# Optimization experiments

Hardware: AMD Instinct MI355X
Metric: run time of the kernel (lower is better)

## Reference

```python
import jax, jax.numpy as jnp
import numpy as np

B, IN, OUT, LAT, HID = 65536, 1, 512, 128, 2048
COEFFS = (IN + 1) * OUT * 2  # (in+1)*out*n_harmonics*n_eig = 2048

def setup_inputs() -> dict:
    key = jax.random.key(0)
    k = jax.random.split(key, 6)
    x = jax.random.normal(k[0], (B, IN + 1 + LAT), dtype=jnp.float32)
    fc1_w = jax.random.normal(k[1], (LAT, HID), dtype=jnp.float32) * (1.0 / np.sqrt(LAT))
    fc1_b = jax.random.normal(k[2], (HID,), dtype=jnp.float32) * 0.02
    fc2_w = jax.random.normal(k[3], (HID, COEFFS), dtype=jnp.float32) * (1.0 / np.sqrt(HID))
    fc2_b = jax.random.normal(k[4], (COEFFS,), dtype=jnp.float32) * 0.02
    dil = jnp.ones((4,), dtype=jnp.float32)      # dilation1..4
    shift_p = jnp.zeros((4,), dtype=jnp.float32)  # shift1..4
    return {"x": x, "fc1_w": fc1_w, "fc1_b": fc1_b, "fc2_w": fc2_w,
            "fc2_b": fc2_b, "dil": dil, "shift_p": shift_p}

def reference(x, fc1_w, fc1_b, fc2_w, fc2_b, dil, shift_p):
    s = x[-1, IN]                       # scalar time of last sample
    inp = x[:, :IN]                     # [B, 1]
    z = x[:, -LAT:]                     # [B, LAT]
    # CoeffDecoder: tanh MLP
    h = jnp.tanh(z @ fc1_w + fc1_b)     # [B, HID]
    coeffs = (h @ fc2_w + fc2_b).reshape(B, (IN + 1) * OUT, 2)
    # aew trig basis Bin (2x4) has only 4 nonzeros; X.sum(2) == coeffs @ Bin.sum(axis=1)
    t = s * dil + shift_p               # [4]
    v = jnp.stack([jnp.cos(t[0]) + jnp.cos(t[2]),
                   jnp.sin(t[1]) + jnp.sin(t[3])])  # [2] = row-sums of Bin
    w = coeffs @ v                      # [B, (IN+1)*OUT]
    weight = w[:, :IN * OUT].reshape(B, IN, OUT)
    bias = w[:, IN * OUT:(IN + 1) * OUT]
    weighted = jnp.einsum('bi,bio->bo', inp, weight)  # bmm([B,1,1],[B,1,OUT]).squeeze(1)
    return weighted + bias              # [B, OUT]
```

## Files before the change

kernel.cpp:

```cpp
#include <hip/hip_runtime.h>
#include <hip/hip_bf16.h>
#include <stddef.h>

#define NB   65536
#define XC   130
#define LATD 128
#define HIDD 2048
#define JC   1024
#define OC   512
#define BAND 16384
#define WBM  256
#define WBN  256
#define BK   64
#define NKT  32

typedef __bf16 bf16_t;
typedef bf16_t bf16x4 __attribute__((ext_vector_type(4)));
typedef bf16_t bf16x8 __attribute__((ext_vector_type(8)));
typedef float  f32x4  __attribute__((ext_vector_type(4)));

typedef __attribute__((address_space(1))) const unsigned char ga_u8;
typedef __attribute__((address_space(3))) unsigned char ls_u8;

__device__ __forceinline__ void dma16(const void* g, void* l) {
  __builtin_amdgcn_global_load_lds((ga_u8*)g, (ls_u8*)l, 16, 0, 0);
}

__global__ void prep_fc1(const float* __restrict__ fc1w, bf16_t* __restrict__ fc1wT) {
  int t = blockIdx.x * blockDim.x + threadIdx.x;
  int k = t & (LATD - 1);
  int n = t >> 7;
  fc1wT[(size_t)n * LATD + k] = (bf16_t)fc1w[(size_t)k * HIDD + n];
}

__global__ void prep_fc2(const float* __restrict__ x, const float* __restrict__ fc2w,
                         const float* __restrict__ fc2b, const float* __restrict__ dil,
                         const float* __restrict__ shp, bf16_t* __restrict__ w2pT,
                         float* __restrict__ b2p) {
  int t = blockIdx.x * blockDim.x + threadIdx.x;
  int k = t & (HIDD - 1);
  int c = t >> 11;
  float s  = x[(size_t)(NB - 1) * XC + 1];
  float t0 = s * dil[0] + shp[0];
  float t1 = s * dil[1] + shp[1];
  float t2 = s * dil[2] + shp[2];
  float t3 = s * dil[3] + shp[3];
  float v0 = cosf(t0) + cosf(t2);
  float v1 = sinf(t1) + sinf(t3);
  int jj = ((c >> 5) * 16 + (c & 15)) + (((c >> 4) & 1) << 9);
  float w0 = fc2w[(size_t)k * 2048 + 2 * jj];
  float w1 = fc2w[(size_t)k * 2048 + 2 * jj + 1];
  w2pT[(size_t)c * HIDD + k] = (bf16_t)(w0 * v0 + w1 * v1);
  if (k == 0) b2p[c] = fc2b[2 * jj] * v0 + fc2b[2 * jj + 1] * v1;
}

__global__ __launch_bounds__(512) void h_kernel(
    const float* __restrict__ x, const float* __restrict__ fc1b,
    const bf16_t* __restrict__ fc1wT, bf16_t* __restrict__ h, int band)
{
  const int t   = threadIdx.x;
  const int w   = t >> 6;
  const int l   = t & 63;
  const int lhi = l >> 4;
  const int llo = l & 15;
  const size_t b0 = (size_t)band * BAND + (size_t)blockIdx.x * 64;
  const int hb  = w & 1;
  const int gb  = (w >> 1) * 16;
  const size_t row_l = (size_t)blockIdx.x * 64 + gb + llo;

  bf16x8 za[4];
  {
    const float* zsrc = x + (b0 + gb + llo) * XC + 2;
#pragma unroll
    for (int ks = 0; ks < 4; ++ks) {
      bf16x8 pk;
#pragma unroll
      for (int i = 0; i < 4; ++i) {
        float2 f = *(const float2*)(zsrc + ks * 32 + lhi * 8 + 2 * i);
        pk[2 * i]     = (bf16_t)f.x;
        pk[2 * i + 1] = (bf16_t)f.y;
      }
      za[ks] = pk;
    }
  }

  auto loadA = [&](bf16x8 (&A)[4], int c) {
    const bf16_t* base = fc1wT + (size_t)(c * 32 + hb * 16 + llo) * LATD + lhi * 8;
#pragma unroll
    for (int ks = 0; ks < 4; ++ks) A[ks] = *(const bf16x8*)(base + ks * 32);
  };
  auto compute = [&](int c, bf16x8 (&A)[4]) {
    f32x4 c1 = {};
#pragma unroll
    for (int ks = 0; ks < 4; ++ks)
      c1 = __builtin_amdgcn_mfma_f32_16x16x32_bf16(A[ks], za[ks], c1, 0, 0, 0);
    float4 fb = *(const float4*)(fc1b + c * 32 + hb * 16 + lhi * 4);
    bf16x4 pk;
#pragma unroll
    for (int r = 0; r < 4; ++r) {
      float pre = c1[r] + ((const float*)&fb)[r];
      float e   = __builtin_amdgcn_exp2f(pre * 2.88539008177792681f);
      float th  = 1.0f - 2.0f * __builtin_amdgcn_rcpf(e + 1.0f);
      pk[r] = (bf16_t)th;
    }
    *(bf16x4*)(h + row_l * HIDD + c * 32 + hb * 16 + lhi * 4) = pk;
  };

  bf16x8 A0[4], A1[4], A2[4], A3[4];
  loadA(A0, 0); loadA(A1, 1); loadA(A2, 2); loadA(A3, 3);
  for (int c = 0; c < 64; c += 4) {
    compute(c,     A0);  loadA(A0, c + 4 < 64 ? c + 4 : 63);
    compute(c + 1, A1);  loadA(A1, c + 5 < 64 ? c + 5 : 63);
    compute(c + 2, A2);  loadA(A2, c + 6 < 64 ? c + 6 : 63);
    compute(c + 3, A3);  loadA(A3, c + 7 < 64 ? c + 7 : 63);
  }
}

__global__ __launch_bounds__(512, 2) void wag_main(
    const float* __restrict__ x, const bf16_t* __restrict__ hband,
    const bf16_t* __restrict__ w2pT, const float* __restrict__ b2p,
    float* __restrict__ out, int band)
{
  __shared__ bf16_t Ab[2][WBM * BK];
  __shared__ bf16_t Bb[2][WBN * BK];
  __shared__ float  inp_lds[WBM];

  const int t   = threadIdx.x;
  const int w   = t >> 6;
  const int l   = t & 63;
  const int lhi = l >> 4;
  const int llo = l & 15;

  const int n   = blockIdx.x;
  const int s_  = n >> 3;
  const int rt  = (n & 7) * 8 + (s_ >> 2);
  const int cg  = s_ & 3;
  const int hr0 = rt * WBM;
  const size_t bg0 = (size_t)band * BAND + hr0;
  const int bc  = cg * WBN;
  const int mrb = (w >> 2) * 128;
  const int ncb = (w & 3) * 64;

  if (t < WBM) inp_lds[t] = x[(bg0 + t) * XC];

  f32x4 acc[8][4] = {};

  auto stageA = [&](int kt) {
    bf16_t* dst = Ab[kt & 1];
#pragma unroll
    for (int q = 0; q < 4; ++q) {
      int idx  = q * 512 + t;
      int row  = idx >> 3, slot = idx & 7;
      const char* src = (const char*)(hband + (size_t)(hr0 + row) * HIDD + kt * BK
                                      + ((slot ^ (row & 7)) * 8));
      dma16(src, (char*)dst + idx * 16);
    }
  };
  auto stageB = [&](int kt) {
    bf16_t* dst = Bb[kt & 1];
#pragma unroll
    for (int q = 0; q < 4; ++q) {
      int idx  = q * 512 + t;
      int col  = idx >> 3, slot = idx & 7;
      const char* src = (const char*)(w2pT + (size_t)(bc + col) * HIDD + kt * BK
                                      + ((slot ^ (col & 7)) * 8));
      dma16(src, (char*)dst + idx * 16);
    }
  };

  auto KSTEP = [&](int kt) {
    const char* Ab_ = (const char*)Ab[kt & 1];
    const char* Bb_ = (const char*)Bb[kt & 1];
#pragma unroll
    for (int ks2 = 0; ks2 < 2; ++ks2) {
      bf16x8 b[4];
#pragma unroll
      for (int j = 0; j < 4; ++j) {
        int col = ncb + j * 16 + llo;
        b[j] = *(const bf16x8*)(Bb_ + col * 128 + ((ks2 * 64 + lhi * 16) ^ ((col & 7) << 4)));
      }
#pragma unroll
      for (int rh = 0; rh < 2; ++rh) {
        bf16x8 a[4];
#pragma unroll
        for (int i = 0; i < 4; ++i) {
          int row = mrb + rh * 64 + i * 16 + llo;
          a[i] = *(const bf16x8*)(Ab_ + row * 128 + ((ks2 * 64 + lhi * 16) ^ ((row & 7) << 4)));
        }
        __builtin_amdgcn_s_setprio(1);
#pragma unroll
        for (int j = 0; j < 4; ++j)
#pragma unroll
          for (int i = 0; i < 4; ++i)
            acc[rh * 4 + i][j] =
                __builtin_amdgcn_mfma_f32_16x16x32_bf16(a[i], b[j], acc[rh * 4 + i][j], 0, 0, 0);
        __builtin_amdgcn_s_setprio(0);
      }
    }
  };

  stageA(0); stageB(0);
  __syncthreads();
  for (int kt = 0; kt < NKT - 1; ++kt) {
    stageA(kt + 1); stageB(kt + 1);
    asm volatile("s_waitcnt vmcnt(8)" ::: "memory");
    __builtin_amdgcn_s_barrier();
    KSTEP(kt);
    asm volatile("s_waitcnt lgkmcnt(0)" ::: "memory");
    __builtin_amdgcn_s_barrier();
  }
  asm volatile("s_waitcnt vmcnt(0)" ::: "memory");
  __builtin_amdgcn_s_barrier();
  KSTEP(NKT - 1);

#pragma unroll
  for (int p = 0; p < 2; ++p) {
    int cw = bc + ncb + p * 32 + llo;
    float bw = b2p[cw];
    float bb = b2p[cw + 16];
    int oc = (bc + ncb + p * 32) / 2 + llo;
#pragma unroll
    for (int fi = 0; fi < 8; ++fi) {
#pragma unroll
      for (int r = 0; r < 4; ++r) {
        int row = mrb + fi * 16 + lhi * 4 + r;
        float wv = acc[fi][2 * p][r] + bw;
        float bv = acc[fi][2 * p + 1][r] + bb;
        out[(bg0 + row) * OC + oc] = inp_lds[row] * wv + bv;
      }
    }
  }
}

extern "C" void kernel_launch(void* const* d_in, const int* in_sizes, int n_in,
                              void* d_out, int out_size, void* d_ws, size_t ws_size,
                              hipStream_t stream) {
  const float* x    = (const float*)d_in[0];
  const float* fc1w = (const float*)d_in[1];
  const float* fc1b = (const float*)d_in[2];
  const float* fc2w = (const float*)d_in[3];
  const float* fc2b = (const float*)d_in[4];
  const float* dil  = (const float*)d_in[5];
  const float* shp  = (const float*)d_in[6];
  float* out = (float*)d_out;

  bf16_t* fc1wT = (bf16_t*)d_ws;
  bf16_t* w2pT  = fc1wT + (size_t)HIDD * LATD;
  float*  b2p   = (float*)(w2pT + (size_t)JC * HIDD);
  bf16_t* hband = (bf16_t*)((char*)d_ws + (8u << 20));

  prep_fc1<<<(HIDD * LATD) / 256, 256, 0, stream>>>(fc1w, fc1wT);
  prep_fc2<<<(JC * HIDD) / 256, 256, 0, stream>>>(x, fc2w, fc2b, dil, shp, w2pT, b2p);

  for (int band = 0; band < NB / BAND; ++band) {
    h_kernel<<<BAND / 64, 512, 0, stream>>>(x, fc1b, fc1wT, hband, band);
    wag_main<<<WBM == 256 ? (BAND / WBM) * (JC / WBN) : 0, 512, 0, stream>>>(
        x, hband, w2pT, b2p, out, band);
  }
}
```

Measured before the change: 570.5 us.

## Coalesce prep_fc2 via LDS transpose and stage h_kernel stores through LDS

prep_fc2 now loads fc2 weight tiles with coalesced reads into shared memory, then transposes them and writes vectorised bf16x8 rows of the folded weight matrix. Previously each thread did strided global reads. h_kernel is reorganised so each block handles 32 rows, and each wave covers a 512-wide slice of the hidden dimension. The tanh outputs go to a per-wave LDS tile first and are then written to global memory as full contiguous 16-byte row segments instead of scattered 8-byte stores. This adds LDS usage and a launch-bounds occupancy hint, and it reloads z for fewer rows per block.

```diff
diff --git a/kernel.cpp b/kernel.cpp
--- a/kernel.cpp
+++ b/kernel.cpp
@@ -33,13 +33,16 @@
   fc1wT[(size_t)n * LATD + k] = (bf16_t)fc1w[(size_t)k * HIDD + n];
 }
 
-__global__ void prep_fc2(const float* __restrict__ x, const float* __restrict__ fc2w,
-                         const float* __restrict__ fc2b, const float* __restrict__ dil,
-                         const float* __restrict__ shp, bf16_t* __restrict__ w2pT,
-                         float* __restrict__ b2p) {
-  int t = blockIdx.x * blockDim.x + threadIdx.x;
-  int k = t & (HIDD - 1);
-  int c = t >> 11;
+__global__ __launch_bounds__(256) void prep_fc2(
+    const float* __restrict__ x, const float* __restrict__ fc2w,
+    const float* __restrict__ fc2b, const float* __restrict__ dil,
+    const float* __restrict__ shp, bf16_t* __restrict__ w2pT,
+    float* __restrict__ b2p) {
+  __shared__ float tile[128 * 67];
+  const int t  = threadIdx.x;
+  const int g  = blockIdx.x;
+  const int k0 = blockIdx.y * 128;
+
   float s  = x[(size_t)(NB - 1) * XC + 1];
   float t0 = s * dil[0] + shp[0];
   float t1 = s * dil[1] + shp[1];
@@ -47,30 +50,58 @@
   float t3 = s * dil[3] + shp[3];
   float v0 = cosf(t0) + cosf(t2);
   float v1 = sinf(t1) + sinf(t3);
-  int jj = ((c >> 5) * 16 + (c & 15)) + (((c >> 4) & 1) << 9);
-  float w0 = fc2w[(size_t)k * 2048 + 2 * jj];
-  float w1 = fc2w[(size_t)k * 2048 + 2 * jj + 1];
-  w2pT[(size_t)c * HIDD + k] = (bf16_t)(w0 * v0 + w1 * v1);
-  if (k == 0) b2p[c] = fc2b[2 * jj] * v0 + fc2b[2 * jj + 1] * v1;
-}
-
-__global__ __launch_bounds__(512) void h_kernel(
+
+  {
+    int fi_ = t & 63, run = fi_ >> 5, fi = fi_ & 31, wv = t >> 6;
+#pragma unroll 8
+    for (int pass = 0; pass < 32; ++pass) {
+      int kr = pass * 4 + wv;
+      tile[kr * 67 + run * 32 + fi] =
+          fc2w[(size_t)(k0 + kr) * 2048 + run * 1024 + g * 32 + fi];
+    }
+  }
+  __syncthreads();
+
+  {
+    int cl = t >> 3, half = (cl >> 4) & 1, col16 = cl & 15;
+    int c = g * 32 + cl;
+    int pb = half * 32 + col16 * 2;
+    bf16x8 ov0, ov1;
+#pragma unroll
+    for (int kk = 0; kk < 16; ++kk) {
+      int k = (t & 7) * 16 + kk;
+      float f0 = tile[k * 67 + pb];
+      float f1 = tile[k * 67 + pb + 1];
+      bf16_t bv = (bf16_t)(f0 * v0 + f1 * v1);
+      if (kk < 8) ov0[kk] = bv; else ov1[kk - 8] = bv;
+    }
+    *(bf16x8*)(w2pT + (size_t)c * 2048 + k0 + (t & 7) * 16)     = ov0;
+    *(bf16x8*)(w2pT + (size_t)c * 2048 + k0 + (t & 7) * 16 + 8) = ov1;
+    if (blockIdx.y == 0 && (t & 7) == 0) {
+      int jj = g * 16 + col16 + (half << 9);
+      b2p[c] = fc2b[2 * jj] * v0 + fc2b[2 * jj + 1] * v1;
+    }
+  }
+}
+
+__global__ __launch_bounds__(512, 4) void h_kernel(
     const float* __restrict__ x, const float* __restrict__ fc1b,
     const bf16_t* __restrict__ fc1wT, bf16_t* __restrict__ h, int band)
 {
+  __shared__ char tile[8][16 * 528];
   const int t   = threadIdx.x;
   const int w   = t >> 6;
   const int l   = t & 63;
   const int lhi = l >> 4;
   const int llo = l & 15;
-  const size_t b0 = (size_t)band * BAND + (size_t)blockIdx.x * 64;
-  const int hb  = w & 1;
-  const int gb  = (w >> 1) * 16;
-  const size_t row_l = (size_t)blockIdx.x * 64 + gb + llo;
+  const size_t b0 = (size_t)band * BAND + (size_t)blockIdx.x * 32;
+  const int rg  = (w & 1) * 16;
+  const int H0  = (w >> 1) * 512;
+  char* tw = tile[w];
 
   bf16x8 za[4];
   {
-    const float* zsrc = x + (b0 + gb + llo) * XC + 2;
+    const float* zsrc = x + (b0 + rg + llo) * XC + 2;
 #pragma unroll
     for (int ks = 0; ks < 4; ++ks) {
       bf16x8 pk;
@@ -84,17 +115,17 @@
     }
   }
 
-  auto loadA = [&](bf16x8 (&A)[4], int c) {
-    const bf16_t* base = fc1wT + (size_t)(c * 32 + hb * 16 + llo) * LATD + lhi * 8;
+  auto loadA = [&](bf16x8 (&A)[4], int cpos) {
+    const bf16_t* base = fc1wT + (size_t)(H0 + cpos * 16 + llo) * LATD + lhi * 8;
 #pragma unroll
     for (int ks = 0; ks < 4; ++ks) A[ks] = *(const bf16x8*)(base + ks * 32);
   };
-  auto compute = [&](int c, bf16x8 (&A)[4]) {
+  auto compute = [&](int cpos, bf16x8 (&A)[4]) {
     f32x4 c1 = {};
 #pragma unroll
     for (int ks = 0; ks < 4; ++ks)
       c1 = __builtin_amdgcn_mfma_f32_16x16x32_bf16(A[ks], za[ks], c1, 0, 0, 0);
-    float4 fb = *(const float4*)(fc1b + c * 32 + hb * 16 + lhi * 4);
+    float4 fb = *(const float4*)(fc1b + H0 + cpos * 16 + lhi * 4);
     bf16x4 pk;
 #pragma unroll
     for (int r = 0; r < 4; ++r) {
@@ -103,16 +134,28 @@
       float th  = 1.0f - 2.0f * __builtin_amdgcn_rcpf(e + 1.0f);
       pk[r] = (bf16_t)th;
     }
-    *(bf16x4*)(h + row_l * HIDD + c * 32 + hb * 16 + lhi * 4) = pk;
-  };
-
-  bf16x8 A0[4], A1[4], A2[4], A3[4];
-  loadA(A0, 0); loadA(A1, 1); loadA(A2, 2); loadA(A3, 3);
-  for (int c = 0; c < 64; c += 4) {
-    compute(c,     A0);  loadA(A0, c + 4 < 64 ? c + 4 : 63);
-    compute(c + 1, A1);  loadA(A1, c + 5 < 64 ? c + 5 : 63);
-    compute(c + 2, A2);  loadA(A2, c + 6 < 64 ? c + 6 : 63);
-    compute(c + 3, A3);  loadA(A3, c + 7 < 64 ? c + 7 : 63);
+    *(bf16x4*)(tw + llo * 528 + (cpos & 15) * 32 + lhi * 8) = pk;
+  };
+
+  for (int half = 0; half < 2; ++half) {
+    bf16x8 A0[4], A1[4];
+    loadA(A0, half * 16 + 0);
+    loadA(A1, half * 16 + 1);
+#pragma unroll
+    for (int nt = 0; nt < 16; nt += 2) {
+      compute(half * 16 + nt, A0);
+      if (nt + 2 < 16) loadA(A0, half * 16 + nt + 2);
+      compute(half * 16 + nt + 1, A1);
+      if (nt + 3 < 16) loadA(A1, half * 16 + nt + 3);
+    }
+#pragma unroll
+    for (int rr = 0; rr < 8; ++rr) {
+      int row = rr * 2 + (l >> 5);
+      int seg = l & 31;
+      bf16x8 v = *(const bf16x8*)(tw + row * 528 + seg * 16);
+      *(bf16x8*)(h + (size_t)(blockIdx.x * 32 + rg + row) * HIDD
+                   + H0 + half * 256 + seg * 8) = v;
+    }
   }
 }
 
@@ -250,11 +293,11 @@
   bf16_t* hband = (bf16_t*)((char*)d_ws + (8u << 20));
 
   prep_fc1<<<(HIDD * LATD) / 256, 256, 0, stream>>>(fc1w, fc1wT);
-  prep_fc2<<<(JC * HIDD) / 256, 256, 0, stream>>>(x, fc2w, fc2b, dil, shp, w2pT, b2p);
+  prep_fc2<<<dim3(32, 16), 256, 0, stream>>>(x, fc2w, fc2b, dil, shp, w2pT, b2p);
 
   for (int band = 0; band < NB / BAND; ++band) {
-    h_kernel<<<BAND / 64, 512, 0, stream>>>(x, fc1b, fc1wT, hband, band);
-    wag_main<<<WBM == 256 ? (BAND / WBM) * (JC / WBN) : 0, 512, 0, stream>>>(
+    h_kernel<<<BAND / 32, 512, 0, stream>>>(x, fc1b, fc1wT, hband, band);
+    wag_main<<<(BAND / WBM) * (JC / WBN), 512, 0, stream>>>(
         x, hband, w2pT, b2p, out, band);
   }
 }
```

Measured after the change: 550.9 us. 3.4% less time.
